# Kernel optimization log

Measured on AMD Instinct MI355X. Metric: run time of the kernel, lower is better.

## Reference

```python
import jax, jax.numpy as jnp
import numpy as np

B, T, I, H = 64, 1024, 256, 512

def setup_inputs() -> dict:
    key = jax.random.key(0)
    ks = jax.random.split(key, 16)
    stdv = 1.0 / np.sqrt(H)
    u = lambda k, shp: jax.random.uniform(k, shp, jnp.float32, -stdv, stdv)
    inp = {"x": jax.random.normal(ks[0], (B, T, I), jnp.float32)}
    names = ["i", "f", "h", "o"]
    for n, g in enumerate(names):
        inp[f"U_{g}"] = u(ks[1 + 3 * n], (I, H))
        inp[f"V_{g}"] = u(ks[2 + 3 * n], (H, H))
        inp[f"b_{g}"] = u(ks[3 + 3 * n], (H,))
    inp["fc_w"] = u(ks[13], (1, H))
    inp["fc_b"] = u(ks[14], (1,))
    return inp

def _lstm_last_h(x, U_i, V_i, b_i, U_f, V_f, b_f, U_h, V_h, b_h, U_o, V_o, b_o):
    # Precompute input projections for all timesteps: [T, B, 4H]
    U = jnp.concatenate([U_i, U_f, U_h, U_o], axis=1)          # [I, 4H]
    b = jnp.concatenate([b_i, b_f, b_h, b_o], axis=0)          # [4H]
    V = jnp.concatenate([V_i, V_f, V_h, V_o], axis=1)          # [H, 4H]
    xproj = jnp.einsum("bti,ig->tbg", x, U) + b                # [T, B, 4H]
    Hn = U_i.shape[1]

    def step(carry, xp_t):
        h, c = carry
        gates = xp_t + h @ V                                   # [B, 4H]
        i_t = jax.nn.sigmoid(gates[:, 0 * Hn:1 * Hn])
        f_t = jax.nn.sigmoid(gates[:, 1 * Hn:2 * Hn])
        g_t = jnp.tanh(gates[:, 2 * Hn:3 * Hn])
        o_t = jax.nn.sigmoid(gates[:, 3 * Hn:4 * Hn])
        c = f_t * c + i_t * g_t
        h = o_t * jnp.tanh(c)
        return (h, c), None

    h0 = jnp.zeros((x.shape[0], Hn), x.dtype)
    c0 = jnp.zeros((x.shape[0], Hn), x.dtype)
    (h_last, _), _ = jax.lax.scan(step, (h0, c0), xproj)
    return h_last

def reference(x, U_i, V_i, b_i, U_f, V_f, b_f, U_h, V_h, b_h, U_o, V_o, b_o, fc_w, fc_b):
    h_last = _lstm_last_h(x, U_i, V_i, b_i, U_f, V_f, b_f, U_h, V_h, b_h, U_o, V_o, b_o)
    return h_last @ fc_w.T + fc_b                              # [B, 1]
```

## Files before the change

### kernel.cpp

```cpp
#include <hip/hip_runtime.h>

typedef _Float16 h8 __attribute__((ext_vector_type(8)));
typedef float    f4 __attribute__((ext_vector_type(4)));
typedef unsigned u4 __attribute__((ext_vector_type(4)));

static const unsigned long long WS_NEEDED = 262144ull;

__device__ __forceinline__ float sigm(float x)   { return 1.0f / (1.0f + __expf(-x)); }
__device__ __forceinline__ float tanh_a(float x) { return 2.0f / (1.0f + __expf(-2.0f * x)) - 1.0f; }

__global__ __launch_bounds__(256) void k_init(unsigned* hbuf)
{
    const int idx = blockIdx.x * 256 + threadIdx.x;
    if (idx < 65536) hbuf[idx] = 0x000003FFu;
}


#define VWAIT0() do { asm volatile("s_waitcnt vmcnt(0)" ::: "memory"); \
                      __builtin_amdgcn_sched_barrier(0); } while (0)
#define LBAR()   do { asm volatile("s_waitcnt lgkmcnt(0)" ::: "memory"); \
                      __builtin_amdgcn_s_barrier(); \
                      __builtin_amdgcn_sched_barrier(0); } while (0)

#define PROBE4() \
    asm volatile( \
        "global_load_dwordx4 %0, %4, off sc0 sc1\n\t" \
        "global_load_dwordx4 %1, %4, off offset:16 sc0 sc1\n\t" \
        "global_load_dwordx4 %2, %4, off offset:1024 sc0 sc1\n\t" \
        "global_load_dwordx4 %3, %4, off offset:1040 sc0 sc1" \
        : "=&v"(qa), "=&v"(qb), "=&v"(qc), "=&v"(qd) \
        : "v"(hp) : "memory")

__device__ __forceinline__ h8 pack8h(u4 a, u4 b)
{
    h8 p;
    p[0] = (_Float16)__uint_as_float(a[0] & 0xFFFFFC00u);
    p[1] = (_Float16)__uint_as_float(a[1] & 0xFFFFFC00u);
    p[2] = (_Float16)__uint_as_float(a[2] & 0xFFFFFC00u);
    p[3] = (_Float16)__uint_as_float(a[3] & 0xFFFFFC00u);
    p[4] = (_Float16)__uint_as_float(b[0] & 0xFFFFFC00u);
    p[5] = (_Float16)__uint_as_float(b[1] & 0xFFFFFC00u);
    p[6] = (_Float16)__uint_as_float(b[2] & 0xFFFFFC00u);
    p[7] = (_Float16)__uint_as_float(b[3] & 0xFFFFFC00u);
    return p;
}
__device__ __forceinline__ h8 pack8f(f4 a, f4 b)
{
    h8 p;
    p[0] = (_Float16)a[0]; p[1] = (_Float16)a[1];
    p[2] = (_Float16)a[2]; p[3] = (_Float16)a[3];
    p[4] = (_Float16)b[0]; p[5] = (_Float16)b[1];
    p[6] = (_Float16)b[2]; p[7] = (_Float16)b[3];
    return p;
}

__global__ __launch_bounds__(256, 1) void k_rec(
    const float* __restrict__ x,
    const float* __restrict__ Ui, const float* __restrict__ Vi, const float* __restrict__ bi,
    const float* __restrict__ Uf, const float* __restrict__ Vf, const float* __restrict__ bf,
    const float* __restrict__ Uh, const float* __restrict__ Vh, const float* __restrict__ bh,
    const float* __restrict__ Uo, const float* __restrict__ Vo, const float* __restrict__ bo,
    unsigned* hbuf)
{
    const int bx = blockIdx.x;
    const int ig = bx & 7;
    const int jg = bx >> 3;
    const int tid = threadIdx.x;
    const int w = tid >> 6, l = tid & 63;
    const int lo = l & 15, hi = l >> 4;
    const int r8 = lo & 7;
    const int unit = jg * 64 + w * 16 + lo;

    __shared__ __align__(16) _Float16 ldsH[2][16 * 32 * 8];
    __shared__ __align__(16) _Float16 ldsX[2][8 * 32 * 8];

    const float* Ug[4] = {Ui, Uf, Uh, Uo};
    const float* Vg[4] = {Vi, Vf, Vh, Vo};
    const float* bg[4] = {bi, bf, bh, bo};

    h8 vfrag[4][16];
    h8 ufrag[4][8];
    float bias[4];
#pragma unroll
    for (int g = 0; g < 4; ++g) {
        bias[g] = bg[g][unit];
#pragma unroll
        for (int kc = 0; kc < 16; ++kc) {
            h8 v;
#pragma unroll
            for (int jj = 0; jj < 8; ++jj)
                v[jj] = (_Float16)Vg[g][(size_t)(kc * 32 + hi * 8 + jj) * 512 + unit];
            vfrag[g][kc] = v;
        }
#pragma unroll
        for (int kc = 0; kc < 8; ++kc) {
            h8 u;
#pragma unroll
            for (int jj = 0; jj < 8; ++jj)
                u[jj] = (_Float16)Ug[g][(size_t)(kc * 32 + hi * 8 + jj) * 512 + unit];
            ufrag[g][kc] = u;
        }
    }

    const int sr = tid >> 5;
    const int sc = (tid & 31) * 8;
    const int kc1 = sc >> 5;
    const int hg1 = (sc >> 3) & 3;
    const int sw1 = ((kc1 & 1) << 2) | hg1;
    const int g1 = kc1 * 32 + hg1 * 8 + (sr ^ sw1);
    const int g2 = (kc1 + 8) * 32 + hg1 * 8 + (sr ^ sw1);

    const float* xrb = x + (size_t)(ig * 8 + sr) * 262144 + sc;

    f4 cst = {0.f, 0.f, 0.f, 0.f};
    f4 xq0, xq1;

    {
        f4 a0, a1;
        asm volatile("global_load_dwordx4 %0, %2, off\n\t"
                     "global_load_dwordx4 %1, %2, off offset:16"
                     : "=&v"(a0), "=&v"(a1) : "v"(xrb) : "memory");
        VWAIT0();
        *(h8*)&ldsX[0][(size_t)g1 * 8] = pack8f(a0, a1);
        const float* xp1 = xrb + 256;
        asm volatile("global_load_dwordx4 %0, %2, off\n\t"
                     "global_load_dwordx4 %1, %2, off offset:16"
                     : "=&v"(xq0), "=&v"(xq1) : "v"(xp1) : "memory");
        LBAR();
    }

    for (int t = 0; t < 1024; ++t) {
        const int pb = t & 1, pn = pb ^ 1;
        const int pr = (t + 1) & 1;
        const unsigned etag = (unsigned)((t + 1023) & 1023);
        const unsigned* hp = hbuf + (size_t)(pr * 8 + ig) * 4096
                                  + (size_t)sr * 512 + sc;

        f4 acc[4], acq[4];
#pragma unroll
        for (int g = 0; g < 4; ++g) {
            f4 a; a[0] = bias[g]; a[1] = bias[g]; a[2] = bias[g]; a[3] = bias[g];
            acc[g] = a;
            f4 z; z[0] = 0.f; z[1] = 0.f; z[2] = 0.f; z[3] = 0.f;
            acq[g] = z;
        }
#pragma unroll
        for (int k = 0; k < 4; ++k) {
            const int ke = 2 * k, ko = 2 * k + 1;
            const int ga = ke * 32 + hi * 8 + (r8 ^ (((ke & 1) << 2) | hi));
            const int gb = ko * 32 + hi * 8 + (r8 ^ (((ko & 1) << 2) | hi));
            const h8 xa = *(const h8*)&ldsX[pb][(size_t)ga * 8];
            const h8 xb = *(const h8*)&ldsX[pb][(size_t)gb * 8];
            acc[0] = __builtin_amdgcn_mfma_f32_16x16x32_f16(xa, ufrag[0][ke], acc[0], 0, 0, 0);
            acc[1] = __builtin_amdgcn_mfma_f32_16x16x32_f16(xa, ufrag[1][ke], acc[1], 0, 0, 0);
            acc[2] = __builtin_amdgcn_mfma_f32_16x16x32_f16(xa, ufrag[2][ke], acc[2], 0, 0, 0);
            acc[3] = __builtin_amdgcn_mfma_f32_16x16x32_f16(xa, ufrag[3][ke], acc[3], 0, 0, 0);
            acq[0] = __builtin_amdgcn_mfma_f32_16x16x32_f16(xb, ufrag[0][ko], acq[0], 0, 0, 0);
            acq[1] = __builtin_amdgcn_mfma_f32_16x16x32_f16(xb, ufrag[1][ko], acq[1], 0, 0, 0);
            acq[2] = __builtin_amdgcn_mfma_f32_16x16x32_f16(xb, ufrag[2][ko], acq[2], 0, 0, 0);
            acq[3] = __builtin_amdgcn_mfma_f32_16x16x32_f16(xb, ufrag[3][ko], acq[3], 0, 0, 0);
        }

        u4 qa, qb, qc, qd;
        PROBE4();

        {
            int tries = 0;
            for (;;) {
                VWAIT0();
                const unsigned m =
                    (qa[0]^etag)|(qa[1]^etag)|(qa[2]^etag)|(qa[3]^etag)|
                    (qb[0]^etag)|(qb[1]^etag)|(qb[2]^etag)|(qb[3]^etag)|
                    (qc[0]^etag)|(qc[1]^etag)|(qc[2]^etag)|(qc[3]^etag)|
                    (qd[0]^etag)|(qd[1]^etag)|(qd[2]^etag)|(qd[3]^etag);
                if ((m & 1023u) == 0u) break;
                if (++tries > 8192) break;
                PROBE4();
            }
        }

        *(h8*)&ldsX[pn][(size_t)g1 * 8] = pack8f(xq0, xq1);
        *(h8*)&ldsH[pb][(size_t)g1 * 8] = pack8h(qa, qb);
        *(h8*)&ldsH[pb][(size_t)g2 * 8] = pack8h(qc, qd);

        {
            const int tn = (t + 2 < 1024) ? t + 2 : 1023;
            const float* xp = xrb + (size_t)tn * 256;
            asm volatile("global_load_dwordx4 %0, %2, off\n\t"
                         "global_load_dwordx4 %1, %2, off offset:16"
                         : "=&v"(xq0), "=&v"(xq1) : "v"(xp) : "memory");
        }

        LBAR();

#pragma unroll
        for (int k = 0; k < 8; ++k) {
            const int kh = k + 8;
            const int ga = k  * 32 + hi * 8 + (r8 ^ (((k  & 1) << 2) | hi));
            const int gb = kh * 32 + hi * 8 + (r8 ^ (((kh & 1) << 2) | hi));
            const h8 a0 = *(const h8*)&ldsH[pb][(size_t)ga * 8];
            const h8 a1 = *(const h8*)&ldsH[pb][(size_t)gb * 8];
            acc[0] = __builtin_amdgcn_mfma_f32_16x16x32_f16(a0, vfrag[0][k],  acc[0], 0, 0, 0);
            acc[1] = __builtin_amdgcn_mfma_f32_16x16x32_f16(a0, vfrag[1][k],  acc[1], 0, 0, 0);
            acc[2] = __builtin_amdgcn_mfma_f32_16x16x32_f16(a0, vfrag[2][k],  acc[2], 0, 0, 0);
            acc[3] = __builtin_amdgcn_mfma_f32_16x16x32_f16(a0, vfrag[3][k],  acc[3], 0, 0, 0);
            acq[0] = __builtin_amdgcn_mfma_f32_16x16x32_f16(a1, vfrag[0][kh], acq[0], 0, 0, 0);
            acq[1] = __builtin_amdgcn_mfma_f32_16x16x32_f16(a1, vfrag[1][kh], acq[1], 0, 0, 0);
            acq[2] = __builtin_amdgcn_mfma_f32_16x16x32_f16(a1, vfrag[2][kh], acq[2], 0, 0, 0);
            acq[3] = __builtin_amdgcn_mfma_f32_16x16x32_f16(a1, vfrag[3][kh], acq[3], 0, 0, 0);
        }

        const unsigned ptag = (unsigned)(t & 1023);
        unsigned pub[4];
#pragma unroll
        for (int d = 0; d < 4; ++d) {
            const float iv = sigm(acc[0][d] + acq[0][d]);
            const float fv = sigm(acc[1][d] + acq[1][d]);
            const float gv = tanh_a(acc[2][d] + acq[2][d]);
            const float ov = sigm(acc[3][d] + acq[3][d]);
            const float c = fv * cst[d] + iv * gv;
            cst[d] = c;
            const float hv = ov * tanh_a(c);
            pub[d] = (__float_as_uint(hv) & 0xFFFFFC00u) | ptag;
        }
        if (hi < 2) {
            unsigned* hw = hbuf + (size_t)((pb * 8 + ig) * 8 + hi * 4) * 512 + unit;
            asm volatile(
                "global_store_dword %4, %0, off sc0 sc1\n\t"
                "global_store_dword %4, %1, off offset:2048 sc0 sc1\n\t"
                "global_store_dword %5, %2, off sc0 sc1\n\t"
                "global_store_dword %5, %3, off offset:2048 sc0 sc1"
                :: "v"(pub[0]), "v"(pub[1]), "v"(pub[2]), "v"(pub[3]),
                   "v"(hw), "v"(hw + 1024)
                : "memory");
        }
    }
}

__global__ __launch_bounds__(64) void k_fc(
    const unsigned* __restrict__ hbuf, const float* __restrict__ fcw,
    const float* __restrict__ fcb, float* __restrict__ out)
{
    const int b = blockIdx.x, l = threadIdx.x;
    const unsigned* h = hbuf + (size_t)((8 + (b >> 3)) * 8 + (b & 7)) * 512;
    float s = 0.f;
#pragma unroll
    for (int k = 0; k < 8; ++k) {
        const float hv = __uint_as_float(h[l + k * 64] & 0xFFFFFC00u);
        s += hv * fcw[l + k * 64];
    }
    for (int off = 32; off > 0; off >>= 1) s += __shfl_down(s, off, 64);
    if (l == 0) out[b] = s + fcb[0];
}

__global__ __launch_bounds__(64) void k_sentinel(float* out)
{
    out[threadIdx.x] = -777777.0f;
}

extern "C" void kernel_launch(void* const* d_in, const int* in_sizes, int n_in,
                              void* d_out, int out_size, void* d_ws, size_t ws_size,
                              hipStream_t stream)
{
    const float* x   = (const float*)d_in[0];
    const float* Ui  = (const float*)d_in[1];
    const float* Vi  = (const float*)d_in[2];
    const float* bi  = (const float*)d_in[3];
    const float* Uf  = (const float*)d_in[4];
    const float* Vf  = (const float*)d_in[5];
    const float* bf  = (const float*)d_in[6];
    const float* Uh  = (const float*)d_in[7];
    const float* Vh  = (const float*)d_in[8];
    const float* bh  = (const float*)d_in[9];
    const float* Uo  = (const float*)d_in[10];
    const float* Vo  = (const float*)d_in[11];
    const float* bo  = (const float*)d_in[12];
    const float* fcw = (const float*)d_in[13];
    const float* fcb = (const float*)d_in[14];
    float* out = (float*)d_out;

    if (ws_size < WS_NEEDED) {
        k_sentinel<<<1, 64, 0, stream>>>(out);
        return;
    }

    unsigned* hbuf = (unsigned*)d_ws;

    k_init<<<256, 256, 0, stream>>>(hbuf);
    k_rec <<<64,  256, 0, stream>>>(x, Ui, Vi, bi, Uf, Vf, bf, Uh, Vh, bh,
                                    Uo, Vo, bo, hbuf);
    k_fc  <<<64,   64, 0, stream>>>(hbuf, fcw, fcb, out);
}
```

Before: 2.707 ms.

## Split recurrent K dimension across wave pairs and double block count

Each workgroup now covers 32 hidden units instead of 64, and the grid doubles to 128 blocks. The two waves sharing a unit group each handle half of the K reduction for the input and recurrent matmuls, then combine partial sums through LDS with an extra barrier. Each wave applies the gate nonlinearities to half the rows. This halves the serial MFMA chain and register fragments per wave, shortening per-step latency. The cost is an extra LDS exchange and barrier each step, and more blocks taking part in the cross-block spin-wait sync.

```diff
diff --git a/kernel.cpp b/kernel.cpp
--- a/kernel.cpp
+++ b/kernel.cpp
@@ -69,36 +69,41 @@
     const int w = tid >> 6, l = tid & 63;
     const int lo = l & 15, hi = l >> 4;
     const int r8 = lo & 7;
-    const int unit = jg * 64 + w * 16 + lo;
+    const int ug = w >> 1;
+    const int khalf = w & 1;
+    const int unit = jg * 32 + ug * 16 + lo;
 
     __shared__ __align__(16) _Float16 ldsH[2][16 * 32 * 8];
     __shared__ __align__(16) _Float16 ldsX[2][8 * 32 * 8];
+    __shared__ __align__(16) f4 ldsP[8 * 128];
 
     const float* Ug[4] = {Ui, Uf, Uh, Uo};
     const float* Vg[4] = {Vi, Vf, Vh, Vo};
     const float* bg[4] = {bi, bf, bh, bo};
 
-    h8 vfrag[4][16];
-    h8 ufrag[4][8];
+    h8 vfrag[4][8];
+    h8 ufrag[4][4];
     float bias[4];
 #pragma unroll
     for (int g = 0; g < 4; ++g) {
-        bias[g] = bg[g][unit];
-#pragma unroll
-        for (int kc = 0; kc < 16; ++kc) {
+        bias[g] = (khalf == 0) ? bg[g][unit] : 0.0f;
+#pragma unroll
+        for (int kk = 0; kk < 8; ++kk) {
+            const int kc = khalf * 8 + kk;
             h8 v;
 #pragma unroll
             for (int jj = 0; jj < 8; ++jj)
                 v[jj] = (_Float16)Vg[g][(size_t)(kc * 32 + hi * 8 + jj) * 512 + unit];
-            vfrag[g][kc] = v;
-        }
-#pragma unroll
-        for (int kc = 0; kc < 8; ++kc) {
+            vfrag[g][kk] = v;
+        }
+#pragma unroll
+        for (int kk = 0; kk < 4; ++kk) {
+            const int kc = khalf * 4 + kk;
             h8 u;
 #pragma unroll
             for (int jj = 0; jj < 8; ++jj)
                 u[jj] = (_Float16)Ug[g][(size_t)(kc * 32 + hi * 8 + jj) * 512 + unit];
-            ufrag[g][kc] = u;
+            ufrag[g][kk] = u;
         }
     }
 
@@ -112,7 +117,7 @@
 
     const float* xrb = x + (size_t)(ig * 8 + sr) * 262144 + sc;
 
-    f4 cst = {0.f, 0.f, 0.f, 0.f};
+    float cst2[2] = {0.f, 0.f};
     f4 xq0, xq1;
 
     {
@@ -144,26 +149,26 @@
             f4 z; z[0] = 0.f; z[1] = 0.f; z[2] = 0.f; z[3] = 0.f;
             acq[g] = z;
         }
-#pragma unroll
-        for (int k = 0; k < 4; ++k) {
-            const int ke = 2 * k, ko = 2 * k + 1;
+        const int kbA = khalf * 4;
+#pragma unroll
+        for (int kk = 0; kk < 2; ++kk) {
+            const int ke = kbA + kk, ko = kbA + 2 + kk;
             const int ga = ke * 32 + hi * 8 + (r8 ^ (((ke & 1) << 2) | hi));
             const int gb = ko * 32 + hi * 8 + (r8 ^ (((ko & 1) << 2) | hi));
             const h8 xa = *(const h8*)&ldsX[pb][(size_t)ga * 8];
             const h8 xb = *(const h8*)&ldsX[pb][(size_t)gb * 8];
-            acc[0] = __builtin_amdgcn_mfma_f32_16x16x32_f16(xa, ufrag[0][ke], acc[0], 0, 0, 0);
-            acc[1] = __builtin_amdgcn_mfma_f32_16x16x32_f16(xa, ufrag[1][ke], acc[1], 0, 0, 0);
-            acc[2] = __builtin_amdgcn_mfma_f32_16x16x32_f16(xa, ufrag[2][ke], acc[2], 0, 0, 0);
-            acc[3] = __builtin_amdgcn_mfma_f32_16x16x32_f16(xa, ufrag[3][ke], acc[3], 0, 0, 0);
-            acq[0] = __builtin_amdgcn_mfma_f32_16x16x32_f16(xb, ufrag[0][ko], acq[0], 0, 0, 0);
-            acq[1] = __builtin_amdgcn_mfma_f32_16x16x32_f16(xb, ufrag[1][ko], acq[1], 0, 0, 0);
-            acq[2] = __builtin_amdgcn_mfma_f32_16x16x32_f16(xb, ufrag[2][ko], acq[2], 0, 0, 0);
-            acq[3] = __builtin_amdgcn_mfma_f32_16x16x32_f16(xb, ufrag[3][ko], acq[3], 0, 0, 0);
+            acc[0] = __builtin_amdgcn_mfma_f32_16x16x32_f16(xa, ufrag[0][kk],     acc[0], 0, 0, 0);
+            acc[1] = __builtin_amdgcn_mfma_f32_16x16x32_f16(xa, ufrag[1][kk],     acc[1], 0, 0, 0);
+            acc[2] = __builtin_amdgcn_mfma_f32_16x16x32_f16(xa, ufrag[2][kk],     acc[2], 0, 0, 0);
+            acc[3] = __builtin_amdgcn_mfma_f32_16x16x32_f16(xa, ufrag[3][kk],     acc[3], 0, 0, 0);
+            acq[0] = __builtin_amdgcn_mfma_f32_16x16x32_f16(xb, ufrag[0][2 + kk], acq[0], 0, 0, 0);
+            acq[1] = __builtin_amdgcn_mfma_f32_16x16x32_f16(xb, ufrag[1][2 + kk], acq[1], 0, 0, 0);
+            acq[2] = __builtin_amdgcn_mfma_f32_16x16x32_f16(xb, ufrag[2][2 + kk], acq[2], 0, 0, 0);
+            acq[3] = __builtin_amdgcn_mfma_f32_16x16x32_f16(xb, ufrag[3][2 + kk], acq[3], 0, 0, 0);
         }
 
         u4 qa, qb, qc, qd;
         PROBE4();
-
         {
             int tries = 0;
             for (;;) {
@@ -182,7 +187,6 @@
         *(h8*)&ldsX[pn][(size_t)g1 * 8] = pack8f(xq0, xq1);
         *(h8*)&ldsH[pb][(size_t)g1 * 8] = pack8h(qa, qb);
         *(h8*)&ldsH[pb][(size_t)g2 * 8] = pack8h(qc, qd);
-
         {
             const int tn = (t + 2 < 1024) ? t + 2 : 1023;
             const float* xp = xrb + (size_t)tn * 256;
@@ -193,45 +197,57 @@
 
         LBAR();
 
-#pragma unroll
-        for (int k = 0; k < 8; ++k) {
-            const int kh = k + 8;
-            const int ga = k  * 32 + hi * 8 + (r8 ^ (((k  & 1) << 2) | hi));
-            const int gb = kh * 32 + hi * 8 + (r8 ^ (((kh & 1) << 2) | hi));
+        const int kbB = khalf * 8;
+#pragma unroll
+        for (int kk = 0; kk < 4; ++kk) {
+            const int ke = kbB + kk, ko = kbB + 4 + kk;
+            const int ga = ke * 32 + hi * 8 + (r8 ^ (((ke & 1) << 2) | hi));
+            const int gb = ko * 32 + hi * 8 + (r8 ^ (((ko & 1) << 2) | hi));
             const h8 a0 = *(const h8*)&ldsH[pb][(size_t)ga * 8];
             const h8 a1 = *(const h8*)&ldsH[pb][(size_t)gb * 8];
-            acc[0] = __builtin_amdgcn_mfma_f32_16x16x32_f16(a0, vfrag[0][k],  acc[0], 0, 0, 0);
-            acc[1] = __builtin_amdgcn_mfma_f32_16x16x32_f16(a0, vfrag[1][k],  acc[1], 0, 0, 0);
-            acc[2] = __builtin_amdgcn_mfma_f32_16x16x32_f16(a0, vfrag[2][k],  acc[2], 0, 0, 0);
-            acc[3] = __builtin_amdgcn_mfma_f32_16x16x32_f16(a0, vfrag[3][k],  acc[3], 0, 0, 0);
-            acq[0] = __builtin_amdgcn_mfma_f32_16x16x32_f16(a1, vfrag[0][kh], acq[0], 0, 0, 0);
-            acq[1] = __builtin_amdgcn_mfma_f32_16x16x32_f16(a1, vfrag[1][kh], acq[1], 0, 0, 0);
-            acq[2] = __builtin_amdgcn_mfma_f32_16x16x32_f16(a1, vfrag[2][kh], acq[2], 0, 0, 0);
-            acq[3] = __builtin_amdgcn_mfma_f32_16x16x32_f16(a1, vfrag[3][kh], acq[3], 0, 0, 0);
-        }
+            acc[0] = __builtin_amdgcn_mfma_f32_16x16x32_f16(a0, vfrag[0][kk],     acc[0], 0, 0, 0);
+            acc[1] = __builtin_amdgcn_mfma_f32_16x16x32_f16(a0, vfrag[1][kk],     acc[1], 0, 0, 0);
+            acc[2] = __builtin_amdgcn_mfma_f32_16x16x32_f16(a0, vfrag[2][kk],     acc[2], 0, 0, 0);
+            acc[3] = __builtin_amdgcn_mfma_f32_16x16x32_f16(a0, vfrag[3][kk],     acc[3], 0, 0, 0);
+            acq[0] = __builtin_amdgcn_mfma_f32_16x16x32_f16(a1, vfrag[0][4 + kk], acq[0], 0, 0, 0);
+            acq[1] = __builtin_amdgcn_mfma_f32_16x16x32_f16(a1, vfrag[1][4 + kk], acq[1], 0, 0, 0);
+            acq[2] = __builtin_amdgcn_mfma_f32_16x16x32_f16(a1, vfrag[2][4 + kk], acq[2], 0, 0, 0);
+            acq[3] = __builtin_amdgcn_mfma_f32_16x16x32_f16(a1, vfrag[3][4 + kk], acq[3], 0, 0, 0);
+        }
+
+        const int p = ug * 64 + l;
+        f4 tot[4];
+#pragma unroll
+        for (int g = 0; g < 4; ++g) {
+            tot[g] = acc[g] + acq[g];
+            ldsP[(khalf * 4 + g) * 128 + p] = tot[g];
+        }
+        LBAR();
+#pragma unroll
+        for (int g = 0; g < 4; ++g)
+            tot[g] = tot[g] + ldsP[((khalf ^ 1) * 4 + g) * 128 + p];
 
         const unsigned ptag = (unsigned)(t & 1023);
-        unsigned pub[4];
-#pragma unroll
-        for (int d = 0; d < 4; ++d) {
-            const float iv = sigm(acc[0][d] + acq[0][d]);
-            const float fv = sigm(acc[1][d] + acq[1][d]);
-            const float gv = tanh_a(acc[2][d] + acq[2][d]);
-            const float ov = sigm(acc[3][d] + acq[3][d]);
-            const float c = fv * cst[d] + iv * gv;
-            cst[d] = c;
+        const int d0 = khalf * 2;
+        unsigned pub2[2];
+#pragma unroll
+        for (int di = 0; di < 2; ++di) {
+            const int d = d0 + di;
+            const float iv = sigm(tot[0][d]);
+            const float fv = sigm(tot[1][d]);
+            const float gv = tanh_a(tot[2][d]);
+            const float ov = sigm(tot[3][d]);
+            const float c = fv * cst2[di] + iv * gv;
+            cst2[di] = c;
             const float hv = ov * tanh_a(c);
-            pub[d] = (__float_as_uint(hv) & 0xFFFFFC00u) | ptag;
+            pub2[di] = (__float_as_uint(hv) & 0xFFFFFC00u) | ptag;
         }
         if (hi < 2) {
-            unsigned* hw = hbuf + (size_t)((pb * 8 + ig) * 8 + hi * 4) * 512 + unit;
+            unsigned* hw = hbuf + (size_t)((pb * 8 + ig) * 8 + hi * 4 + d0) * 512 + unit;
             asm volatile(
-                "global_store_dword %4, %0, off sc0 sc1\n\t"
-                "global_store_dword %4, %1, off offset:2048 sc0 sc1\n\t"
-                "global_store_dword %5, %2, off sc0 sc1\n\t"
-                "global_store_dword %5, %3, off offset:2048 sc0 sc1"
-                :: "v"(pub[0]), "v"(pub[1]), "v"(pub[2]), "v"(pub[3]),
-                   "v"(hw), "v"(hw + 1024)
+                "global_store_dword %2, %0, off sc0 sc1\n\t"
+                "global_store_dword %2, %1, off offset:2048 sc0 sc1"
+                :: "v"(pub2[0]), "v"(pub2[1]), "v"(hw)
                 : "memory");
         }
     }
@@ -287,7 +303,7 @@
     unsigned* hbuf = (unsigned*)d_ws;
 
     k_init<<<256, 256, 0, stream>>>(hbuf);
-    k_rec <<<64,  256, 0, stream>>>(x, Ui, Vi, bi, Uf, Vf, bf, Uh, Vh, bh,
+    k_rec <<<128, 256, 0, stream>>>(x, Ui, Vi, bi, Uf, Vf, bf, Uh, Vh, bh,
                                     Uo, Vo, bo, hbuf);
     k_fc  <<<64,   64, 0, stream>>>(hbuf, fcw, fcb, out);
 }
```

New measurement: 2.379 ms. 1.14x faster.
